# Kernel optimization log

Measured on AMD Instinct MI355X. Metric: run time of the kernel, lower is better.

The kernel has to match this reference:

```python
import jax, jax.numpy as jnp
import numpy as np

B, L, C, NH = 512, 196, 384, 12
HW = 14  # window side

def _relative_position_index(h, w):
    coords = np.stack(np.meshgrid(np.arange(h), np.arange(w), indexing='ij'))  # [2,h,w]
    cf = coords.reshape(2, -1)                       # [2, L]
    rel = cf[:, :, None] - cf[:, None, :]            # [2, L, L]
    rel = rel.transpose(1, 2, 0).astype(np.int64)    # [L, L, 2]
    rel[..., 0] += h - 1
    rel[..., 1] += w - 1
    rel[..., 0] *= 2 * w - 1
    return rel.sum(-1)                               # [L, L]

def setup_inputs() -> dict:
    key = jax.random.key(0)
    ks = jax.random.split(key, 5)
    hd = C // NH
    x = jax.random.normal(ks[0], (B, L, C), dtype=jnp.float32)
    # weights stored as [in, out] (equivalent to torch Linear weight.T)
    qkv_w = jax.random.normal(ks[1], (C, 3 * C), dtype=jnp.float32) * (C ** -0.5)
    qkv_b = jnp.zeros((3 * C,), dtype=jnp.float32)
    proj_w = jax.random.normal(ks[2], (C, C), dtype=jnp.float32) * (C ** -0.5)
    proj_b = jnp.zeros((C,), dtype=jnp.float32)
    bias_table = jax.random.normal(ks[3], ((2 * HW - 1) ** 2, NH), dtype=jnp.float32) * 0.02
    rel_index = jnp.asarray(_relative_position_index(HW, HW), dtype=jnp.int32)
    return {"x": x, "qkv_w": qkv_w, "qkv_b": qkv_b, "proj_w": proj_w,
            "proj_b": proj_b, "bias_table": bias_table, "rel_index": rel_index}

def reference(x, qkv_w, qkv_b, proj_w, proj_b, bias_table, rel_index):
    b, l, c = x.shape
    nh = bias_table.shape[1]
    hd = c // nh
    scale = hd ** -0.5
    qkv = (x @ qkv_w + qkv_b).reshape(b, l, 3, nh, hd).transpose(2, 0, 3, 1, 4)  # [3,B,nh,L,hd]
    q, k, v = qkv[0] * scale, qkv[1], qkv[2]
    attn = jnp.einsum('bhqd,bhkd->bhqk', q, k)                 # [B,nh,L,L]
    bias = bias_table[rel_index]                               # [L,L,nh]
    attn = attn + bias.transpose(2, 0, 1)[None]                # add [1,nh,L,L]
    attn = jax.nn.softmax(attn, axis=-1)
    out = jnp.einsum('bhqk,bhkd->bhqd', attn, v)               # [B,nh,L,hd]
    out = out.transpose(0, 2, 1, 3).reshape(b, l, c)
    return out @ proj_w + proj_b
```

## Files before the change

### kernel.cpp

```cpp
#include <hip/hip_runtime.h>
#include <hip/hip_bf16.h>
#include <stdint.h>

typedef __hip_bfloat16 bf16;
typedef __attribute__((ext_vector_type(8))) short frag8;
typedef __attribute__((ext_vector_type(4))) float floatx4;

#define B_WIN 512
#define L_TOK 196
#define C_DIM 384
#define NH    12
#define HD    32
#define QP    208
#define KPAD  224
#define VSTR  232
#define QSCALE 0.2550348555f

#if defined(__has_builtin)
#if __has_builtin(__builtin_amdgcn_exp2f)
#define EXP2(x) __builtin_amdgcn_exp2f(x)
#endif
#endif
#ifndef EXP2
#define EXP2(x) exp2f(x)
#endif

__device__ __forceinline__ void async_cp16(const void* g, void* l) {
  __builtin_amdgcn_global_load_lds(
      (const __attribute__((address_space(1))) unsigned int*)g,
      (__attribute__((address_space(3))) unsigned int*)l, 16, 0, 0);
}

__device__ __forceinline__ unsigned short f2bf_bits(float f) {
  bf16 b = __float2bfloat16(f);
  return *(unsigned short*)&b;
}

__global__ void cast_to_bf16(const float* __restrict__ src, bf16* __restrict__ dst) {
  int i = blockIdx.x * 256 + threadIdx.x;
  float4 v = ((const float4*)src)[i];
  ushort4 o;
  o.x = f2bf_bits(v.x); o.y = f2bf_bits(v.y);
  o.z = f2bf_bits(v.z); o.w = f2bf_bits(v.w);
  ((ushort4*)dst)[i] = o;
}

__global__ void transpose_cast(const float* __restrict__ src, bf16* __restrict__ dst,
                               int K, int N) {
  int idx = blockIdx.x * 256 + threadIdx.x;
  if (idx >= K * N) return;
  int k = idx / N, n = idx - k * N;
  dst[n * K + k] = __float2bfloat16(src[idx]);
}

__global__ void bias_fill(const float* __restrict__ table, const int* __restrict__ rel,
                          float* __restrict__ biasf) {
  int idx = blockIdx.x * 256 + threadIdx.x;
  int h = idx / (QP * KPAD);
  int rem = idx - h * (QP * KPAD);
  int q = rem / KPAD, j = rem - q * KPAD;
  int t = j >> 4, qd = (j >> 2) & 3, rr = j & 3;
  int k = (t >> 1) * 32 + qd * 8 + (t & 1) * 4 + rr;
  float v;
  if (q >= L_TOK)      v = 0.f;
  else if (k >= L_TOK) v = -1e30f;
  else                 v = table[rel[q * L_TOK + k] * NH + h] * 1.4426950408889634f;
  biasf[idx] = v;
}

__device__ __forceinline__ void storev(bf16* p, float v)  { *p = __float2bfloat16(v); }
__device__ __forceinline__ void storev(float* p, float v) { *p = v; }

template <typename OT>
__global__ __launch_bounds__(256) void gemm_bt(
    const bf16* __restrict__ A, const bf16* __restrict__ Bt,
    const float* __restrict__ bias, OT* __restrict__ C,
    int M, int N, int K, int lda, int qcols, int nbn, int panel) {
  __shared__ __align__(16) bf16 sA[2][128 * 32];
  __shared__ __align__(16) bf16 sB[2][128 * 32];
  const int tid = threadIdx.x;
  const int wave = tid >> 6, lane = tid & 63;
  const int SUPER = panel * nbn;
  const int bid = blockIdx.x;
  const int sb = bid / SUPER, rsp = bid - sb * SUPER;
  const long bm = (long)(sb * panel + rsp % panel) * 128;
  const long bn = (long)(rsp / panel) * 128;

  const int srow = wave * 32 + (lane >> 2);
  const int scol = (lane & 3) * 8;
  const bf16* gA = A + (bm + srow) * (long)lda + scol;
  const bf16* gB = Bt + (bn + srow) * (long)K + scol;

  floatx4 acc[4][4];
#pragma unroll
  for (int i = 0; i < 4; i++)
#pragma unroll
    for (int j = 0; j < 4; j++) acc[i][j] = (floatx4)(0.f);

  const int wr = (wave & 1) * 64;
  const int wc = (wave >> 1) * 64;

#pragma unroll
  for (int j = 0; j < 2; j++) {
    async_cp16(gA + (size_t)j * 16 * lda, &sA[0][(wave * 32 + j * 16) * 32]);
    async_cp16(gB + (size_t)j * 16 * K, &sB[0][(wave * 32 + j * 16) * 32]);
  }
  __syncthreads();

  int cur = 0;
  for (int k0 = 0; k0 < K; k0 += 32) {
    if (k0 + 32 < K) {
#pragma unroll
      for (int j = 0; j < 2; j++) {
        async_cp16(gA + (size_t)j * 16 * lda + (k0 + 32),
                   &sA[cur ^ 1][(wave * 32 + j * 16) * 32]);
        async_cp16(gB + (size_t)j * 16 * K + (k0 + 32),
                   &sB[cur ^ 1][(wave * 32 + j * 16) * 32]);
      }
    }
    frag8 af[4], bfr[4];
#pragma unroll
    for (int mi = 0; mi < 4; mi++)
      af[mi] = *(const frag8*)&sA[cur][(wr + mi * 16 + (lane & 15)) * 32 + (lane >> 4) * 8];
#pragma unroll
    for (int ni = 0; ni < 4; ni++)
      bfr[ni] = *(const frag8*)&sB[cur][(wc + ni * 16 + (lane & 15)) * 32 + (lane >> 4) * 8];
#pragma unroll
    for (int mi = 0; mi < 4; mi++)
#pragma unroll
      for (int ni = 0; ni < 4; ni++)
        acc[mi][ni] = __builtin_amdgcn_mfma_f32_16x16x32_bf16(af[mi], bfr[ni], acc[mi][ni], 0, 0, 0);
    __syncthreads();
    cur ^= 1;
  }

#pragma unroll
  for (int ni = 0; ni < 4; ni++) {
    const long col = bn + wc + ni * 16 + (lane & 15);
    const float bv = bias[col];
#pragma unroll
    for (int mi = 0; mi < 4; mi++)
#pragma unroll
      for (int r = 0; r < 4; r++) {
        const long row = bm + wr + mi * 16 + (lane >> 4) * 4 + r;
        float val = acc[mi][ni][r] + bv;
        if (col < qcols) val *= QSCALE;
        storev(&C[row * N + col], val);
      }
  }
}

__global__ __launch_bounds__(256, 4) void attn_win(
    bf16* __restrict__ qkv, const float* __restrict__ biasf) {
  __shared__ __align__(16) bf16 kL[KPAD * 32];
  __shared__ __align__(16) bf16 vT[HD * VSTR];
  const int b = blockIdx.x, h = blockIdx.y;
  const int tid = threadIdx.x, wave = tid >> 6, lane = tid & 63;
  bf16* base = qkv + (size_t)b * L_TOK * (3 * C_DIM);

  const int colb = lane & 15;
  const int quad = lane >> 4;
  const int rsub = quad * 4;
  const int kswz = (quad ^ ((colb >> 1) & 3)) * 8;

  const bf16* vbase = base + 2 * C_DIM + h * HD;
  const int i0 = tid;
  const int r0a = i0 >> 2, c8a = (i0 & 3) * 8;
  const bf16* ga = vbase + (size_t)(2 * r0a) * (3 * C_DIM) + c8a;
  uint4 a0 = *(const uint4*)ga;
  uint4 a1 = *(const uint4*)(ga + 3 * C_DIM);
  const int i1 = tid + 256;
  const bool h1 = i1 < 392;
  const int r0b = h1 ? (i1 >> 2) : r0a, c8b = h1 ? (i1 & 3) * 8 : c8a;
  const bf16* gb = vbase + (size_t)(2 * r0b) * (3 * C_DIM) + c8b;
  uint4 b0 = make_uint4(0, 0, 0, 0), b1 = make_uint4(0, 0, 0, 0);
  if (h1) { b0 = *(const uint4*)gb; b1 = *(const uint4*)(gb + 3 * C_DIM); }

  for (int c = wave; c < 14; c += 4) {
    const int j = c * 16 + (lane >> 2);
    const int slot = lane & 3;
    const int t = j >> 4, qd = (j >> 2) & 3, rr = j & 3;
    int k = (t >> 1) * 32 + qd * 8 + (t & 1) * 4 + rr;
    if (k > L_TOK - 1) k = L_TOK - 1;
    const int sj = (j >> 1) & 3;
    const bf16* src = base + (size_t)k * (3 * C_DIM) + C_DIM + h * HD + ((slot ^ sj) * 8);
    async_cp16(src, &kL[c * 512]);
  }

  frag8 aqv[4];
#pragma unroll
  for (int i = 0; i < 4; i++) {
    int rg = wave + 4 * i; if (rg > 12) rg = 12;
    int qrow = rg * 16 + colb; if (qrow > L_TOK - 1) qrow = L_TOK - 1;
    aqv[i] = *(const frag8*)(base + (size_t)qrow * (3 * C_DIM) + h * HD + quad * 8);
  }

  const float* bB = biasf + (size_t)h * QP * KPAD;
  floatx4 s[14];
#pragma unroll
  for (int t = 0; t < 14; t++)
    s[t] = *(const floatx4*)(bB + (size_t)(wave * 16 + colb) * KPAD + t * 16 + rsub);

  {
    ushort ea0[8], ea1[8];
    *(uint4*)ea0 = a0; *(uint4*)ea1 = a1;
#pragma unroll
    for (int e = 0; e < 8; e++) {
      uint32_t pack = (uint32_t)ea0[e] | ((uint32_t)ea1[e] << 16);
      *(uint32_t*)&vT[(c8a + e) * VSTR + 2 * r0a] = pack;
    }
    if (h1) {
      ushort eb0[8], eb1[8];
      *(uint4*)eb0 = b0; *(uint4*)eb1 = b1;
#pragma unroll
      for (int e = 0; e < 8; e++) {
        uint32_t pack = (uint32_t)eb0[e] | ((uint32_t)eb1[e] << 16);
        *(uint32_t*)&vT[(c8b + e) * VSTR + 2 * r0b] = pack;
      }
    }
  }
  for (int idx = tid; idx < HD * 14; idx += 256) {
    int d = idx / 14, pr = idx - d * 14;
    *(uint32_t*)&vT[d * VSTR + L_TOK + 2 * pr] = 0;
  }
  __syncthreads();

#pragma unroll
  for (int ii = 0; ii < 4; ii++) {
    const int rg = wave + 4 * ii;
    if (rg < 13) {
      const int row0 = rg * 16;
      const bool pre = (rg + 4 < 13);

#pragma unroll
      for (int t = 0; t < 14; t++) {
        const frag8 bk = *(const frag8*)&kL[(t * 16 + colb) * 32 + kswz];
        s[t] = __builtin_amdgcn_mfma_f32_16x16x32_bf16(bk, aqv[ii], s[t], 0, 0, 0);
      }

      float lsum = 0.f;
#pragma unroll
      for (int t = 0; t < 14; t++)
#pragma unroll
        for (int r = 0; r < 4; r++) {
          float p = EXP2(s[t][r]);
          s[t][r] = p;
          lsum += p;
        }
      lsum += __shfl_xor(lsum, 16, 64);
      lsum += __shfl_xor(lsum, 32, 64);
      const float rl = 1.0f / lsum;
      float rln[4];
#pragma unroll
      for (int r = 0; r < 4; r++) rln[r] = __shfl(rl, rsub + r, 64);

      const float* bBn = bB + (size_t)(row0 + 64 + colb) * KPAD;
      floatx4 o[2] = {(floatx4)(0.f), (floatx4)(0.f)};
#pragma unroll
      for (int kk = 0; kk < 7; kk++) {
        frag8 ap;
#pragma unroll
        for (int e = 0; e < 4; e++) ap[e] = (short)f2bf_bits(s[2 * kk][e]);
#pragma unroll
        for (int e = 0; e < 4; e++) ap[4 + e] = (short)f2bf_bits(s[2 * kk + 1][e]);
        if (pre) {
          s[2 * kk]     = *(const floatx4*)(bBn + (2 * kk) * 16 + rsub);
          s[2 * kk + 1] = *(const floatx4*)(bBn + (2 * kk + 1) * 16 + rsub);
        }
#pragma unroll
        for (int nt = 0; nt < 2; nt++) {
          const frag8 bv = *(const frag8*)&vT[(nt * 16 + colb) * VSTR + kk * 32 + quad * 8];
          o[nt] = __builtin_amdgcn_mfma_f32_16x16x32_bf16(ap, bv, o[nt], 0, 0, 0);
        }
      }
#pragma unroll
      for (int nt = 0; nt < 2; nt++)
#pragma unroll
        for (int r = 0; r < 4; r++) {
          const int grow = row0 + rsub + r;
          if (grow < L_TOK)
            base[(size_t)grow * (3 * C_DIM) + h * HD + nt * 16 + colb] =
                __float2bfloat16(o[nt][r] * rln[r]);
        }
    }
  }
}

extern "C" void kernel_launch(void* const* d_in, const int* in_sizes, int n_in,
                              void* d_out, int out_size, void* d_ws, size_t ws_size,
                              hipStream_t stream) {
  const float* x      = (const float*)d_in[0];
  const float* qkv_w  = (const float*)d_in[1];
  const float* qkv_b  = (const float*)d_in[2];
  const float* proj_w = (const float*)d_in[3];
  const float* proj_b = (const float*)d_in[4];
  const float* btab   = (const float*)d_in[5];
  const int*   relidx = (const int*)d_in[6];
  float* out = (float*)d_out;

  const size_t M = (size_t)B_WIN * L_TOK;
  char* ws = (char*)d_ws;
  size_t off = 0;
  bf16*  qkv   = (bf16*)(ws + off);  off += M * 1152 * 2;
  bf16*  wT1   = (bf16*)(ws + off);  off += (size_t)1152 * 384 * 2;
  bf16*  wT2   = (bf16*)(ws + off);  off += (size_t)384 * 384 * 2;
  float* biasf = (float*)(ws + off); off += (size_t)NH * QP * KPAD * 4;

  bf16* xb = (bf16*)d_out;

  cast_to_bf16<<<(int)(M * C_DIM / 4 / 256), 256, 0, stream>>>(x, xb);
  transpose_cast<<<(384 * 1152 + 255) / 256, 256, 0, stream>>>(qkv_w, wT1, 384, 1152);
  transpose_cast<<<(384 * 384 + 255) / 256, 256, 0, stream>>>(proj_w, wT2, 384, 384);
  bias_fill<<<(NH * QP * KPAD) / 256, 256, 0, stream>>>(btab, relidx, biasf);

  gemm_bt<bf16><<<784 * 9, 256, 0, stream>>>(xb, wT1, qkv_b, qkv,
                                             (int)M, 1152, 384, 384, C_DIM, 9, 56);
  attn_win<<<dim3(B_WIN, NH), 256, 0, stream>>>(qkv, biasf);
  gemm_bt<float><<<784 * 3, 256, 0, stream>>>(qkv, wT2, proj_b, out,
                                              (int)M, 384, 384, 1152, 0, 3, 56);
}
```

Baseline: 637.6 us.

## Stream score tiles through softmax to cut registers, repad V, retune GEMM grouping

The attention kernel no longer holds all 14 score accumulators plus prefetched bias in registers. It computes each pair of QK tiles, adds bias loaded just in time, exponentiates, and packs straight into bf16 P fragments. This lowers register pressure, and the launch-bounds occupancy hint is dropped. The V transpose stride is changed to alter LDS bank mapping, the bf16 x copy moves into workspace when it fits, and the GEMM swizzle group parameter is halved. The cost is that bias loads are no longer prefetched ahead of the QK MFMAs, which may expose more load latency.

After: 638.2 us. No clear change (+0.1%).

```diff
diff --git a/kernel.cpp b/kernel.cpp
--- a/kernel.cpp
+++ b/kernel.cpp
@@ -13,7 +13,7 @@
 #define HD    32
 #define QP    208
 #define KPAD  224
-#define VSTR  232
+#define VSTR  236
 #define QSCALE 0.2550348555f
 
 #if defined(__has_builtin)
@@ -150,7 +150,7 @@
   }
 }
 
-__global__ __launch_bounds__(256, 4) void attn_win(
+__global__ __launch_bounds__(256) void attn_win(
     bf16* __restrict__ qkv, const float* __restrict__ biasf) {
   __shared__ __align__(16) bf16 kL[KPAD * 32];
   __shared__ __align__(16) bf16 vT[HD * VSTR];
@@ -195,12 +195,6 @@
     aqv[i] = *(const frag8*)(base + (size_t)qrow * (3 * C_DIM) + h * HD + quad * 8);
   }
 
-  const float* bB = biasf + (size_t)h * QP * KPAD;
-  floatx4 s[14];
-#pragma unroll
-  for (int t = 0; t < 14; t++)
-    s[t] = *(const floatx4*)(bB + (size_t)(wave * 16 + colb) * KPAD + t * 16 + rsub);
-
   {
     ushort ea0[8], ea1[8];
     *(uint4*)ea0 = a0; *(uint4*)ea1 = a1;
@@ -225,28 +219,38 @@
   }
   __syncthreads();
 
+  const float* bB = biasf + (size_t)h * QP * KPAD;
+
 #pragma unroll
   for (int ii = 0; ii < 4; ii++) {
     const int rg = wave + 4 * ii;
     if (rg < 13) {
       const int row0 = rg * 16;
-      const bool pre = (rg + 4 < 13);
-
-#pragma unroll
-      for (int t = 0; t < 14; t++) {
-        const frag8 bk = *(const frag8*)&kL[(t * 16 + colb) * 32 + kswz];
-        s[t] = __builtin_amdgcn_mfma_f32_16x16x32_bf16(bk, aqv[ii], s[t], 0, 0, 0);
+      const float* bR = bB + (size_t)(row0 + colb) * KPAD;
+
+      frag8 ap[7];
+      float lsum = 0.f;
+#pragma unroll
+      for (int kk = 0; kk < 7; kk++) {
+        const floatx4 b0v = *(const floatx4*)(bR + (2 * kk) * 16 + rsub);
+        const floatx4 b1v = *(const floatx4*)(bR + (2 * kk + 1) * 16 + rsub);
+        const frag8 k0 = *(const frag8*)&kL[((2 * kk) * 16 + colb) * 32 + kswz];
+        const frag8 k1 = *(const frag8*)&kL[((2 * kk + 1) * 16 + colb) * 32 + kswz];
+        floatx4 s0 = __builtin_amdgcn_mfma_f32_16x16x32_bf16(k0, aqv[ii], (floatx4)(0.f), 0, 0, 0);
+        floatx4 s1 = __builtin_amdgcn_mfma_f32_16x16x32_bf16(k1, aqv[ii], (floatx4)(0.f), 0, 0, 0);
+#pragma unroll
+        for (int e = 0; e < 4; e++) {
+          float p = EXP2(s0[e] + b0v[e]);
+          lsum += p;
+          ap[kk][e] = (short)f2bf_bits(p);
+        }
+#pragma unroll
+        for (int e = 0; e < 4; e++) {
+          float p = EXP2(s1[e] + b1v[e]);
+          lsum += p;
+          ap[kk][4 + e] = (short)f2bf_bits(p);
+        }
       }
-
-      float lsum = 0.f;
-#pragma unroll
-      for (int t = 0; t < 14; t++)
-#pragma unroll
-        for (int r = 0; r < 4; r++) {
-          float p = EXP2(s[t][r]);
-          s[t][r] = p;
-          lsum += p;
-        }
       lsum += __shfl_xor(lsum, 16, 64);
       lsum += __shfl_xor(lsum, 32, 64);
       const float rl = 1.0f / lsum;
@@ -254,25 +258,14 @@
 #pragma unroll
       for (int r = 0; r < 4; r++) rln[r] = __shfl(rl, rsub + r, 64);
 
-      const float* bBn = bB + (size_t)(row0 + 64 + colb) * KPAD;
       floatx4 o[2] = {(floatx4)(0.f), (floatx4)(0.f)};
 #pragma unroll
-      for (int kk = 0; kk < 7; kk++) {
-        frag8 ap;
-#pragma unroll
-        for (int e = 0; e < 4; e++) ap[e] = (short)f2bf_bits(s[2 * kk][e]);
-#pragma unroll
-        for (int e = 0; e < 4; e++) ap[4 + e] = (short)f2bf_bits(s[2 * kk + 1][e]);
-        if (pre) {
-          s[2 * kk]     = *(const floatx4*)(bBn + (2 * kk) * 16 + rsub);
-          s[2 * kk + 1] = *(const floatx4*)(bBn + (2 * kk + 1) * 16 + rsub);
-        }
+      for (int kk = 0; kk < 7; kk++)
 #pragma unroll
         for (int nt = 0; nt < 2; nt++) {
           const frag8 bv = *(const frag8*)&vT[(nt * 16 + colb) * VSTR + kk * 32 + quad * 8];
-          o[nt] = __builtin_amdgcn_mfma_f32_16x16x32_bf16(ap, bv, o[nt], 0, 0, 0);
+          o[nt] = __builtin_amdgcn_mfma_f32_16x16x32_bf16(ap[kk], bv, o[nt], 0, 0, 0);
         }
-      }
 #pragma unroll
       for (int nt = 0; nt < 2; nt++)
 #pragma unroll
@@ -306,7 +299,8 @@
   bf16*  wT2   = (bf16*)(ws + off);  off += (size_t)384 * 384 * 2;
   float* biasf = (float*)(ws + off); off += (size_t)NH * QP * KPAD * 4;
 
-  bf16* xb = (bf16*)d_out;
+  bf16* xb = (ws_size >= off + M * C_DIM * sizeof(bf16))
+                 ? (bf16*)(ws + off) : (bf16*)d_out;
 
   cast_to_bf16<<<(int)(M * C_DIM / 4 / 256), 256, 0, stream>>>(x, xb);
   transpose_cast<<<(384 * 1152 + 255) / 256, 256, 0, stream>>>(qkv_w, wT1, 384, 1152);
@@ -314,8 +308,8 @@
   bias_fill<<<(NH * QP * KPAD) / 256, 256, 0, stream>>>(btab, relidx, biasf);
 
   gemm_bt<bf16><<<784 * 9, 256, 0, stream>>>(xb, wT1, qkv_b, qkv,
-                                             (int)M, 1152, 384, 384, C_DIM, 9, 56);
+                                             (int)M, 1152, 384, 384, C_DIM, 9, 28);
   attn_win<<<dim3(B_WIN, NH), 256, 0, stream>>>(qkv, biasf);
   gemm_bt<float><<<784 * 3, 256, 0, stream>>>(qkv, wT2, proj_b, out,
-                                              (int)M, 384, 384, 1152, 0, 3, 56);
-}
+                                              (int)M, 384, 384, 1152, 0, 3, 28);
+}
```
